# Optimization experiments

Measured on AMD Instinct MI355X. Metric: run time of the kernel, lower is better.

Reference implementation:

```python
import jax, jax.numpy as jnp
import numpy as np

BN_EPS = 1e-5

def conv1x1(w, b, x):
    # w: [O, C], b: [O], x: [B, C, H, W] -> [B, O, H, W]
    return jnp.einsum('oc,bchw->bohw', w, x) + b[None, :, None, None]

def setup_inputs() -> dict:
    key = jax.random.key(0)
    ks = jax.random.split(key, 11)
    C, inter = 256, 128
    B, H, W = 16, 64, 32
    s = 0.05
    return {
        'x': jax.random.normal(ks[0], (B, C, H, W), jnp.float32),
        'g_w': jax.random.normal(ks[1], (inter, C), jnp.float32) * s,
        'g_b': jax.random.normal(ks[2], (inter,), jnp.float32) * s,
        'theta_w': jax.random.normal(ks[3], (inter, C), jnp.float32) * s,
        'theta_b': jax.random.normal(ks[4], (inter,), jnp.float32) * s,
        'phi_w': jax.random.normal(ks[5], (inter, C), jnp.float32) * s,
        'phi_b': jax.random.normal(ks[6], (inter,), jnp.float32) * s,
        'W_w': jax.random.normal(ks[7], (C, inter), jnp.float32) * s,
        'W_b': jax.random.normal(ks[8], (C,), jnp.float32) * s,
        'bn_gamma': jax.random.normal(ks[9], (C,), jnp.float32) * s,
        'bn_beta': jax.random.normal(ks[10], (C,), jnp.float32) * s,
    }

def reference(x, g_w, g_b, theta_w, theta_b, phi_w, phi_b, W_w, W_b, bn_gamma, bn_beta):
    B, C, H, W = x.shape
    N = H * W
    inter = g_w.shape[0]
    # 1x1 conv projections, flattened to token sequences
    g_x = conv1x1(g_w, g_b, x).reshape(B, inter, N).transpose(0, 2, 1)        # [B, N, inter]
    theta_x = conv1x1(theta_w, theta_b, x).reshape(B, inter, N).transpose(0, 2, 1)  # [B, N, inter]
    phi_x = conv1x1(phi_w, phi_b, x).reshape(B, inter, N)                      # [B, inter, N]
    # non-local attention: f = theta @ phi / N, then y = f @ g
    f_div_c = jnp.einsum('bnd,bdm->bnm', theta_x, phi_x) / N                   # [B, N, N]
    y = jnp.einsum('bnm,bmd->bnd', f_div_c, g_x)                               # [B, N, inter]
    y = y.transpose(0, 2, 1).reshape(B, inter, H, W)
    # W: 1x1 conv + BatchNorm (training-mode batch statistics)
    z = conv1x1(W_w, W_b, y)                                                   # [B, C, H, W]
    mean = jnp.mean(z, axis=(0, 2, 3), keepdims=True)
    var = jnp.var(z, axis=(0, 2, 3), keepdims=True)
    z_hat = (z - mean) * jax.lax.rsqrt(var + BN_EPS)
    z_bn = z_hat * bn_gamma[None, :, None, None] + bn_beta[None, :, None, None]
    return z_bn + x
```

## Files before the change

kernel.cpp:

```cpp
#include <hip/hip_runtime.h>

typedef unsigned int uint;
typedef unsigned short ushort;
typedef __attribute__((ext_vector_type(8))) short bf16x8;
typedef __attribute__((ext_vector_type(4))) float f32x4;

#define BB 16
#define CC 256
#define II 128
#define NN 2048
#define BN_EPS 1e-5f

#define OFF_GPART 0
#define OFF_SPART 8388608
#define OFF_GPT   8421376
#define OFF_CP    8425472
#define OFF_STATP 8429568
#define OFF_STAT2 8560640
#define OFF_PT    8561152
#define OFF_R1    8561408
#define OFF_WGB   8561664
#define OFF_ALPHA 8561920
#define OFF_L1    8562176
#define OFF_R2    8566272
#define OFF_FEND  8570368
#define UGRAM 0
#define UE    1048576
#define UFT   1114112
#define USBF  1179648
#define UXT   2228224
#define UZ    10616832

static __device__ __forceinline__ ushort f2bf(float f) {
    uint u = __float_as_uint(f);
    return (ushort)((u + 0x7FFFu + ((u >> 16) & 1u)) >> 16);
}
static __device__ __forceinline__ uint pack2(float a, float b) {
    return (uint)f2bf(a) | ((uint)f2bf(b) << 16);
}
static __device__ __forceinline__ float bflo(uint w) { return __uint_as_float(w << 16); }
static __device__ __forceinline__ float bfhi(uint w) { return __uint_as_float(w & 0xFFFF0000u); }

#define MICRO_FMA(av, bv) \
    acc[0][0] += av.x * bv.x; acc[0][1] += av.x * bv.y; acc[0][2] += av.x * bv.z; acc[0][3] += av.x * bv.w; \
    acc[1][0] += av.y * bv.x; acc[1][1] += av.y * bv.y; acc[1][2] += av.y * bv.z; acc[1][3] += av.y * bv.w; \
    acc[2][0] += av.z * bv.x; acc[2][1] += av.z * bv.y; acc[2][2] += av.z * bv.z; acc[2][3] += av.z * bv.w; \
    acc[3][0] += av.w * bv.x; acc[3][1] += av.w * bv.y; acc[3][2] += av.w * bv.z; acc[3][3] += av.w * bv.w;

__global__ __launch_bounds__(256) void mega1(
    const float* __restrict__ x,
    const float* __restrict__ Ww, const float* __restrict__ Gw,
    const float* __restrict__ Pw, const float* __restrict__ Tw,
    const float* __restrict__ gb, const float* __restrict__ pb, const float* __restrict__ tb,
    float* __restrict__ gpart, float* __restrict__ sPart, ushort* __restrict__ xT,
    ushort* __restrict__ EBF, ushort* __restrict__ FT,
    float* __restrict__ pt, float* __restrict__ r1, float* __restrict__ wgb,
    float* __restrict__ alpha)
{
    __shared__ __align__(16) char smem[20480];
    const int bid = blockIdx.x;
    const int t = threadIdx.x;

    if (bid < 512) {
        ushort (*As)[40] = (ushort(*)[40])smem;
        ushort (*Bs)[40] = (ushort(*)[40])(smem + 10240);
        const int jt = bid & 1, it = (bid >> 1) & 1;
        const int z = bid >> 2;
        const int b = z >> 3, kc = z & 7;
        const int iBase = it * 128, jBase = jt * 128;
        const bool diag = (it == jt);
        const int arow = t >> 1, ah = t & 1;
        const float* aSrc = x + ((size_t)(b * CC + iBase + arow)) * NN + kc * 256 + ah * 16;
        const float* bSrc = x + ((size_t)(b * CC + jBase + arow)) * NN + kc * 256 + ah * 16;
        const int lane = t & 63, wid = t >> 6;
        const int mb = (wid >> 1) * 64, nb = (wid & 1) * 64;
        const int lm = lane & 15, q = lane >> 4;
        f32x4 acc[4][4] = {};
        float ssum = 0.f;

        for (int it16 = 0; it16 < 8; ++it16) {
            const float4* ap = (const float4*)(aSrc + it16 * 32);
            float4 a0 = ap[0], a1 = ap[1], a2 = ap[2], a3 = ap[3];
            uint4 pa0 = { pack2(a0.x,a0.y), pack2(a0.z,a0.w), pack2(a1.x,a1.y), pack2(a1.z,a1.w) };
            uint4 pa1 = { pack2(a2.x,a2.y), pack2(a2.z,a2.w), pack2(a3.x,a3.y), pack2(a3.z,a3.w) };
            *(uint4*)&As[arow][ah * 16]     = pa0;
            *(uint4*)&As[arow][ah * 16 + 8] = pa1;
            if (!diag) {
                const float4* bp = (const float4*)(bSrc + it16 * 32);
                float4 b0 = bp[0], b1 = bp[1], b2 = bp[2], b3 = bp[3];
                uint4 pb0 = { pack2(b0.x,b0.y), pack2(b0.z,b0.w), pack2(b1.x,b1.y), pack2(b1.z,b1.w) };
                uint4 pb1 = { pack2(b2.x,b2.y), pack2(b2.z,b2.w), pack2(b3.x,b3.y), pack2(b3.z,b3.w) };
                *(uint4*)&Bs[arow][ah * 16]     = pb0;
                *(uint4*)&Bs[arow][ah * 16 + 8] = pb1;
            }
            if (jt == 0) {
                ssum += a0.x+a0.y+a0.z+a0.w + a1.x+a1.y+a1.z+a1.w
                      + a2.x+a2.y+a2.z+a2.w + a3.x+a3.y+a3.z+a3.w;
            }
            __syncthreads();
            const ushort (*Bsel)[40] = diag ? (const ushort(*)[40])As : (const ushort(*)[40])Bs;
            bf16x8 af[4], bf[4];
            #pragma unroll
            for (int mt = 0; mt < 4; ++mt)
                af[mt] = *(const bf16x8*)&As[mb + mt * 16 + lm][q * 8];
            #pragma unroll
            for (int nt = 0; nt < 4; ++nt)
                bf[nt] = *(const bf16x8*)&Bsel[nb + nt * 16 + lm][q * 8];
            #pragma unroll
            for (int mt = 0; mt < 4; ++mt)
                #pragma unroll
                for (int nt = 0; nt < 4; ++nt)
                    acc[mt][nt] = __builtin_amdgcn_mfma_f32_16x16x32_bf16(af[mt], bf[nt], acc[mt][nt], 0, 0, 0);
            if (diag) {
                const int n_l = t & 31, cg = t >> 5;
                uint qv[8];
                #pragma unroll
                for (int i2 = 0; i2 < 8; ++i2) {
                    ushort lo = As[cg * 16 + 2*i2][n_l];
                    ushort hi = As[cg * 16 + 2*i2 + 1][n_l];
                    qv[i2] = (uint)lo | ((uint)hi << 16);
                }
                const int ng = kc * 256 + it16 * 32 + n_l;
                uint4* op = (uint4*)(xT + ((size_t)(b * NN + ng)) * CC + iBase + cg * 16);
                op[0] = make_uint4(qv[0], qv[1], qv[2], qv[3]);
                op[1] = make_uint4(qv[4], qv[5], qv[6], qv[7]);
            }
            __syncthreads();
        }
        float* gp = gpart + ((size_t)kc * BB + b) * CC * CC;
        #pragma unroll
        for (int mt = 0; mt < 4; ++mt)
            #pragma unroll
            for (int nt = 0; nt < 4; ++nt)
                #pragma unroll
                for (int r = 0; r < 4; ++r) {
                    const int gi = iBase + mb + mt * 16 + q * 4 + r;
                    const int gj = jBase + nb + nt * 16 + lm;
                    gp[(size_t)gi * CC + gj] = acc[mt][nt][r];
                }
        if (jt == 0) {
            const float so = __shfl_xor(ssum, 1);
            if ((t & 1) == 0)
                sPart[((size_t)kc * BB + b) * CC + iBase + arow] = ssum + so;
        }
        return;
    }

    const int bz = bid - 512;
    if (bz == 32) {
        float ptv = 0.f, r1v = 0.f, wgbv = 0.f;
        for (int d = 0; d < II; ++d) {
            ptv  += Pw[(size_t)d * CC + t] * tb[d];
            r1v  += Tw[(size_t)d * CC + t] * pb[d];
            wgbv += Ww[(size_t)t * II + d] * gb[d];
        }
        pt[t] = ptv; r1[t] = r1v; wgb[t] = wgbv;
        if (t == 0) {
            float al = 0.f;
            for (int d = 0; d < II; ++d) al += pb[d] * tb[d];
            alpha[0] = al;
        }
        return;
    }
    float (*As)[68] = (float(*)[68])smem;
    float (*Bs)[68] = (float(*)[68])(smem + 8704);
    const int a_r = t >> 2, a_k = (t & 3) * 8;
    const int b_n = t & 63, b_k = t >> 6;
    const int ty = t >> 4, tx = t & 15;
    float acc[4][4] = {};
    if (bz < 16) {
        const int cBase = (bz >> 2) * 64, iBase = (bz & 3) * 64;
        const float* ap0 = Ww + (size_t)(cBase + a_r) * II + a_k;
        const float* bp0 = Gw + iBase + b_n;
        for (int k0 = 0; k0 < II; k0 += 32) {
            #pragma unroll
            for (int j = 0; j < 8; ++j) As[a_k + j][a_r] = ap0[k0 + j];
            #pragma unroll
            for (int kk = 0; kk < 8; ++kk) {
                const int k = b_k + kk * 4;
                Bs[k][b_n] = bp0[(size_t)(k0 + k) * CC];
            }
            __syncthreads();
            #pragma unroll
            for (int k = 0; k < 32; ++k) {
                const float4 av = *(const float4*)&As[k][ty * 4];
                const float4 bv = *(const float4*)&Bs[k][tx * 4];
                MICRO_FMA(av, bv)
            }
            __syncthreads();
        }
        #pragma unroll
        for (int ii = 0; ii < 4; ++ii) {
            uint2 o = { pack2(acc[ii][0], acc[ii][1]), pack2(acc[ii][2], acc[ii][3]) };
            *(uint2*)&EBF[(size_t)(cBase + ty * 4 + ii) * CC + iBase + tx * 4] = o;
        }
    } else {
        const int zz = bz - 16;
        const int jBase = (zz >> 2) * 64, kBase = (zz & 3) * 64;
        const float* ap0 = Tw + jBase + b_n;
        const float* bp0 = Pw + kBase + b_n;
        for (int k0 = 0; k0 < II; k0 += 32) {
            #pragma unroll
            for (int kk = 0; kk < 8; ++kk) {
                const int k = b_k + kk * 4;
                As[k][b_n] = ap0[(size_t)(k0 + k) * CC];
                Bs[k][b_n] = bp0[(size_t)(k0 + k) * CC];
            }
            __syncthreads();
            #pragma unroll
            for (int k = 0; k < 32; ++k) {
                const float4 av = *(const float4*)&As[k][ty * 4];
                const float4 bv = *(const float4*)&Bs[k][tx * 4];
                MICRO_FMA(av, bv)
            }
            __syncthreads();
        }
        const float sc = 1.0f / (float)NN;
        #pragma unroll
        for (int ii = 0; ii < 4; ++ii) {
            uint2 o = { pack2(acc[ii][0]*sc, acc[ii][1]*sc), pack2(acc[ii][2]*sc, acc[ii][3]*sc) };
            *(uint2*)&FT[(size_t)(jBase + ty * 4 + ii) * CC + kBase + tx * 4] = o;
        }
    }
}

__global__ __launch_bounds__(256) void mega2(
    const float* __restrict__ gpart, const float* __restrict__ pt,
    ushort* __restrict__ GramBF, float* __restrict__ Gpt)
{
    __shared__ float ptL[256];
    const int bid = blockIdx.x;
    const int t = threadIdx.x;
    const int i = bid * 256 + t;
    const size_t S = (size_t)BB * CC * CC / 4;
    const float4* p = (const float4*)gpart;
    if (t < 256) ptL[t] = pt[t];
    float4 o = { 0.f, 0.f, 0.f, 0.f };
    #pragma unroll
    for (int k = 0; k < 8; ++k) {
        float4 v = p[i + (size_t)k * S];
        o.x += v.x; o.y += v.y; o.z += v.z; o.w += v.w;
    }
    uint2 pk = { pack2(o.x, o.y), pack2(o.z, o.w) };
    ((uint2*)GramBF)[i] = pk;
    __syncthreads();
    const int lane = t & 63;
    float dot = o.x * ptL[lane * 4] + o.y * ptL[lane * 4 + 1]
              + o.z * ptL[lane * 4 + 2] + o.w * ptL[lane * 4 + 3];
    #pragma unroll
    for (int m = 32; m > 0; m >>= 1) dot += __shfl_xor(dot, m);
    if (lane == 0) {
        const int row = bid * 4 + (t >> 6);
        Gpt[row] = dot;
    }
}

__global__ __launch_bounds__(256) void u_kernel(
    const float* __restrict__ sPart, const float* __restrict__ Gpt,
    const ushort* __restrict__ EBF, const ushort* __restrict__ FT,
    const float* __restrict__ pt, const float* __restrict__ r1,
    const float* __restrict__ wgb, const float* __restrict__ alpha,
    float* __restrict__ cprime, float* __restrict__ L1, float* __restrict__ R2)
{
    const int b = blockIdx.x, t = threadIdx.x;
    __shared__ __align__(16) float sL[256], GptL[256], red[256];
    {
        float s = 0.f;
        #pragma unroll
        for (int kc = 0; kc < 8; ++kc) s += sPart[((size_t)kc * BB + b) * CC + t];
        sL[t] = s;
        GptL[t] = Gpt[b * CC + t];
        red[t] = s * pt[t];
    }
    __syncthreads();
    for (int s = 128; s > 0; s >>= 1) {
        if (t < s) red[t] += red[t + s];
        __syncthreads();
    }
    const float spt = red[0];
    float es = 0.f, eg = 0.f;
    {
        const uint4* ep = (const uint4*)(EBF + (size_t)t * CC);
        #pragma unroll 4
        for (int kk = 0; kk < 32; ++kk) {
            uint4 v = ep[kk]; const int k = kk * 8;
            float e0=bflo(v.x),e1=bfhi(v.x),e2=bflo(v.y),e3=bfhi(v.y);
            float e4=bflo(v.z),e5=bfhi(v.z),e6=bflo(v.w),e7=bfhi(v.w);
            es += e0*sL[k]+e1*sL[k+1]+e2*sL[k+2]+e3*sL[k+3]+e4*sL[k+4]+e5*sL[k+5]+e6*sL[k+6]+e7*sL[k+7];
            eg += e0*GptL[k]+e1*GptL[k+1]+e2*GptL[k+2]+e3*GptL[k+3]+e4*GptL[k+4]+e5*GptL[k+5]+e6*GptL[k+6]+e7*GptL[k+7];
        }
    }
    float r2 = 0.f;
    {
        const uint4* fp = (const uint4*)(FT + (size_t)t * CC);
        #pragma unroll 4
        for (int kk = 0; kk < 32; ++kk) {
            uint4 v = fp[kk]; const int k = kk * 8;
            r2 += bflo(v.x)*sL[k]   + bfhi(v.x)*sL[k+1] + bflo(v.y)*sL[k+2] + bfhi(v.y)*sL[k+3]
                + bflo(v.z)*sL[k+4] + bfhi(v.z)*sL[k+5] + bflo(v.w)*sL[k+6] + bfhi(v.w)*sL[k+7];
        }
    }
    const float al = alpha[0];
    const float wg = wgb[t];
    cprime[b * CC + t] = (eg + al * es + spt * wg) / (float)NN + al * wg;
    L1[b * CC + t] = es / (float)NN;
    R2[b * CC + t] = r2 + r1[t];
}

__global__ __launch_bounds__(256) void sfused(
    const ushort* __restrict__ EBF, const ushort* __restrict__ GramBF,
    const ushort* __restrict__ FT,
    const float* __restrict__ r1, const float* __restrict__ R2,
    const float* __restrict__ L1, const float* __restrict__ wgb,
    ushort* __restrict__ Sbf)
{
    __shared__ ushort As[128][40];
    __shared__ ushort Bs[128][40];
    __shared__ ushort Qs[128][264];
    const int t = threadIdx.x;
    const int b = blockIdx.x >> 2;
    const int ct = (blockIdx.x >> 1) & 1, jt = blockIdx.x & 1;
    const int cBase = ct * 128, jBase = jt * 128;
    const int arow = t >> 1, ah = t & 1;
    const int lane = t & 63, wid = t >> 6;
    const int mb = (wid >> 1) * 64, nb = (wid & 1) * 64;
    const int lm = lane & 15, q = lane >> 4;
    const ushort* aSrc = EBF + (size_t)(cBase + arow) * CC + ah * 16;

    #pragma unroll
    for (int half = 0; half < 2; ++half) {
        const ushort* bSrc = GramBF + ((size_t)b * CC + half * 128 + arow) * CC + ah * 16;
        f32x4 acc[4][4] = {};
        for (int k0 = 0; k0 < CC; k0 += 32) {
            *(uint4*)&As[arow][ah * 16]     = ((const uint4*)(aSrc + k0))[0];
            *(uint4*)&As[arow][ah * 16 + 8] = ((const uint4*)(aSrc + k0))[1];
            *(uint4*)&Bs[arow][ah * 16]     = ((const uint4*)(bSrc + k0))[0];
            *(uint4*)&Bs[arow][ah * 16 + 8] = ((const uint4*)(bSrc + k0))[1];
            __syncthreads();
            bf16x8 af[4], bf[4];
            #pragma unroll
            for (int mt = 0; mt < 4; ++mt)
                af[mt] = *(const bf16x8*)&As[mb + mt * 16 + lm][q * 8];
            #pragma unroll
            for (int nt = 0; nt < 4; ++nt)
                bf[nt] = *(const bf16x8*)&Bs[nb + nt * 16 + lm][q * 8];
            #pragma unroll
            for (int mt = 0; mt < 4; ++mt)
                #pragma unroll
                for (int nt = 0; nt < 4; ++nt)
                    acc[mt][nt] = __builtin_amdgcn_mfma_f32_16x16x32_bf16(af[mt], bf[nt], acc[mt][nt], 0, 0, 0);
            __syncthreads();
        }
        #pragma unroll
        for (int mt = 0; mt < 4; ++mt)
            #pragma unroll
            for (int nt = 0; nt < 4; ++nt)
                #pragma unroll
                for (int r = 0; r < 4; ++r)
                    Qs[mb + mt * 16 + q * 4 + r][half * 128 + nb + nt * 16 + lm] = f2bf(acc[mt][nt][r]);
        __syncthreads();
    }
    f32x4 acc[4][4] = {};
    const ushort* fSrc = FT + (size_t)(jBase + arow) * CC + ah * 16;
    for (int k0 = 0; k0 < CC; k0 += 32) {
        *(uint4*)&Bs[arow][ah * 16]     = ((const uint4*)(fSrc + k0))[0];
        *(uint4*)&Bs[arow][ah * 16 + 8] = ((const uint4*)(fSrc + k0))[1];
        __syncthreads();
        bf16x8 af[4], bf[4];
        #pragma unroll
        for (int mt = 0; mt < 4; ++mt)
            af[mt] = *(const bf16x8*)&Qs[mb + mt * 16 + lm][k0 + q * 8];
        #pragma unroll
        for (int nt = 0; nt < 4; ++nt)
            bf[nt] = *(const bf16x8*)&Bs[nb + nt * 16 + lm][q * 8];
        #pragma unroll
        for (int mt = 0; mt < 4; ++mt)
            #pragma unroll
            for (int nt = 0; nt < 4; ++nt)
                acc[mt][nt] = __builtin_amdgcn_mfma_f32_16x16x32_bf16(af[mt], bf[nt], acc[mt][nt], 0, 0, 0);
        __syncthreads();
    }
    float r1v[4], R2v[4];
    #pragma unroll
    for (int nt = 0; nt < 4; ++nt) {
        const int j = jBase + nb + nt * 16 + lm;
        r1v[nt] = r1[j];
        R2v[nt] = R2[b * CC + j];
    }
    ushort* dst = Sbf + (size_t)b * CC * CC;
    #pragma unroll
    for (int mt = 0; mt < 4; ++mt)
        #pragma unroll
        for (int r = 0; r < 4; ++r) {
            const int c = cBase + mb + mt * 16 + q * 4 + r;
            const float l1v = L1[b * CC + c], wgv = wgb[c];
            #pragma unroll
            for (int nt = 0; nt < 4; ++nt) {
                const int j = jBase + nb + nt * 16 + lm;
                dst[(size_t)c * CC + j] = f2bf(acc[mt][nt][r] + l1v * r1v[nt] + wgv * R2v[nt]);
            }
        }
}

__global__ __launch_bounds__(256) void z_mfma(
    const ushort* __restrict__ Sbf, const ushort* __restrict__ xT,
    const float* __restrict__ cprime, ushort* __restrict__ zbf,
    float* __restrict__ statsPart)
{
    __shared__ ushort As[128][40];
    __shared__ ushort Bs[128][40];
    __shared__ float cpL[128];
    __shared__ float sSum[2][128], sSq[2][128];
    const int t = threadIdx.x;
    const int n0 = blockIdx.x * 128, ct = blockIdx.y * 128, b = blockIdx.z;
    const int arow = t >> 1, ah = t & 1;
    const ushort* aSrc = Sbf + ((size_t)(b * CC + ct + arow)) * CC + ah * 16;
    const ushort* bSrc = xT + ((size_t)(b * NN + n0 + arow)) * CC + ah * 16;
    const int lane = t & 63, wid = t >> 6;
    const int mb = (wid >> 1) * 64, nb = (wid & 1) * 64;
    const int lm = lane & 15, q = lane >> 4;
    f32x4 acc[4][4] = {};

    if (t < 128) cpL[t] = cprime[b * CC + ct + t];

    for (int k0 = 0; k0 < CC; k0 += 32) {
        *(uint4*)&As[arow][ah * 16]     = ((const uint4*)(aSrc + k0))[0];
        *(uint4*)&As[arow][ah * 16 + 8] = ((const uint4*)(aSrc + k0))[1];
        *(uint4*)&Bs[arow][ah * 16]     = ((const uint4*)(bSrc + k0))[0];
        *(uint4*)&Bs[arow][ah * 16 + 8] = ((const uint4*)(bSrc + k0))[1];
        __syncthreads();
        bf16x8 af[4], bf[4];
        #pragma unroll
        for (int mt = 0; mt < 4; ++mt)
            af[mt] = *(const bf16x8*)&As[mb + mt * 16 + lm][q * 8];
        #pragma unroll
        for (int nt = 0; nt < 4; ++nt)
            bf[nt] = *(const bf16x8*)&Bs[nb + nt * 16 + lm][q * 8];
        #pragma unroll
        for (int mt = 0; mt < 4; ++mt)
            #pragma unroll
            for (int nt = 0; nt < 4; ++nt)
                acc[mt][nt] = __builtin_amdgcn_mfma_f32_16x16x32_bf16(af[mt], bf[nt], acc[mt][nt], 0, 0, 0);
        __syncthreads();
    }
    const int nbw = wid & 1;
    #pragma unroll
    for (int mt = 0; mt < 4; ++mt) {
        #pragma unroll
        for (int r = 0; r < 4; ++r) {
            const int cl = mb + mt * 16 + q * 4 + r;
            const int ci = ct + cl;
            const float cp = cpL[cl];
            const size_t zrow = ((size_t)(b * CC + ci)) * NN;
            float s1 = 0.f, q1 = 0.f;
            #pragma unroll
            for (int nt = 0; nt < 4; ++nt) {
                const float val = acc[mt][nt][r] + cp;
                const int tok = n0 + nb + nt * 16 + lm;
                zbf[zrow + tok] = f2bf(val);
                s1 += val; q1 += val * val;
            }
            #pragma unroll
            for (int m = 1; m < 16; m <<= 1) {
                s1 += __shfl_xor(s1, m);
                q1 += __shfl_xor(q1, m);
            }
            if (lm == 0) { sSum[nbw][cl] = s1; sSq[nbw][cl] = q1; }
        }
    }
    __syncthreads();
    if (t < 128) {
        const int slot = blockIdx.z * 16 + blockIdx.x;
        statsPart[(size_t)slot * 512 + ct + t]       = sSum[0][t] + sSum[1][t];
        statsPart[(size_t)slot * 512 + 256 + ct + t] = sSq[0][t] + sSq[1][t];
    }
}

__global__ __launch_bounds__(512) void bn_finalize(
    const float* __restrict__ statsPart, float* __restrict__ stats2)
{
    __shared__ float red[4][128];
    __shared__ float sf[128];
    const int g = blockIdx.x;
    const int t = threadIdx.x;
    const int cl = t & 127, sg = t >> 7;
    const int col = (cl < 64) ? (g * 64 + cl) : (256 + g * 64 + (cl - 64));
    float a = 0.f;
    for (int s = sg * 64; s < sg * 64 + 64; ++s)
        a += statsPart[(size_t)s * 512 + col];
    red[sg][cl] = a;
    __syncthreads();
    if (t < 128) sf[t] = red[0][t] + red[1][t] + red[2][t] + red[3][t];
    __syncthreads();
    if (t < 64) {
        const float cnt = (float)(BB * NN);
        const float mean = sf[t] / cnt;
        const float var = sf[64 + t] / cnt - mean * mean;
        const int c = g * 64 + t;
        stats2[c] = mean;
        stats2[CC + c] = rsqrtf(var + BN_EPS);
    }
}

__global__ __launch_bounds__(256) void bn_apply(
    const ushort* __restrict__ zbf, const float* __restrict__ x,
    float* __restrict__ out, const float* __restrict__ stats2,
    const float* __restrict__ gamma, const float* __restrict__ beta)
{
    const size_t i = (size_t)blockIdx.x * 256 + threadIdx.x;
    const size_t base = i * 8;
    const int c = (int)((base >> 11) & (CC - 1));
    const float mean = stats2[c], istd = stats2[CC + c];
    const float gm = gamma[c] * istd;
    const float bt = beta[c] - mean * gm;
    const uint4 zz = *(const uint4*)(zbf + base);
    const float4 x0 = *(const float4*)(x + base);
    const float4 x1 = *(const float4*)(x + base + 4);
    float4 o0, o1;
    o0.x = bflo(zz.x) * gm + bt + x0.x;  o0.y = bfhi(zz.x) * gm + bt + x0.y;
    o0.z = bflo(zz.y) * gm + bt + x0.z;  o0.w = bfhi(zz.y) * gm + bt + x0.w;
    o1.x = bflo(zz.z) * gm + bt + x1.x;  o1.y = bfhi(zz.z) * gm + bt + x1.y;
    o1.z = bflo(zz.w) * gm + bt + x1.z;  o1.w = bfhi(zz.w) * gm + bt + x1.w;
    *(float4*)(out + base) = o0;
    *(float4*)(out + base + 4) = o1;
}

extern "C" void kernel_launch(void* const* d_in, const int* in_sizes, int n_in,
                              void* d_out, int out_size, void* d_ws, size_t ws_size,
                              hipStream_t stream) {
    const float* x    = (const float*)d_in[0];
    const float* g_w  = (const float*)d_in[1];
    const float* g_b  = (const float*)d_in[2];
    const float* th_w = (const float*)d_in[3];
    const float* th_b = (const float*)d_in[4];
    const float* ph_w = (const float*)d_in[5];
    const float* ph_b = (const float*)d_in[6];
    const float* W_w  = (const float*)d_in[7];
    const float* bn_g = (const float*)d_in[9];
    const float* bn_bt= (const float*)d_in[10];
    float* wsf = (float*)d_ws;
    float* out = (float*)d_out;
    ushort* ub = (ushort*)(wsf + OFF_FEND);

    mega1<<<dim3(545), 256, 0, stream>>>(
        x, W_w, g_w, ph_w, th_w, g_b, ph_b, th_b,
        wsf + OFF_GPART, wsf + OFF_SPART, ub + UXT,
        ub + UE, ub + UFT,
        wsf + OFF_PT, wsf + OFF_R1, wsf + OFF_WGB, wsf + OFF_ALPHA);
    mega2<<<dim3(1024), 256, 0, stream>>>(
        wsf + OFF_GPART, wsf + OFF_PT, ub + UGRAM, wsf + OFF_GPT);
    u_kernel<<<dim3(16), 256, 0, stream>>>(
        wsf + OFF_SPART, wsf + OFF_GPT, ub + UE, ub + UFT,
        wsf + OFF_PT, wsf + OFF_R1, wsf + OFF_WGB, wsf + OFF_ALPHA,
        wsf + OFF_CP, wsf + OFF_L1, wsf + OFF_R2);
    sfused<<<dim3(64), 256, 0, stream>>>(
        ub + UE, ub + UGRAM, ub + UFT,
        wsf + OFF_R1, wsf + OFF_R2, wsf + OFF_L1, wsf + OFF_WGB, ub + USBF);
    z_mfma<<<dim3(16, 2, 16), 256, 0, stream>>>(
        ub + USBF, ub + UXT, wsf + OFF_CP, ub + UZ, wsf + OFF_STATP);
    bn_finalize<<<dim3(4), 512, 0, stream>>>(wsf + OFF_STATP, wsf + OFF_STAT2);
    bn_apply<<<dim3(4096), 256, 0, stream>>>(ub + UZ, x, out, wsf + OFF_STAT2, bn_g, bn_bt);
}
```

Baseline: 193.8 us.

## Double-buffer LDS tiles and prefetch next K-slice into registers in Gram and z GEMMs

The Gram-matrix phase of mega1 and the z_mfma kernel now use two LDS buffers and load the next K-slice from global memory into registers while the current slice is consumed by MFMA. The trailing barrier per iteration is removed and replaced by a single barrier that waits only on LDS counters, so global loads can stay in flight across it. This is meant to hide global-load latency behind compute. The cost is double the shared memory (40 KB in mega1), which may reduce occupancy.

```diff
diff --git a/kernel.cpp b/kernel.cpp
--- a/kernel.cpp
+++ b/kernel.cpp
@@ -10,6 +10,8 @@
 #define II 128
 #define NN 2048
 #define BN_EPS 1e-5f
+
+#define SYNC_LDS() { __builtin_amdgcn_s_waitcnt(0xC07F); __builtin_amdgcn_s_barrier(); }
 
 #define OFF_GPART 0
 #define OFF_SPART 8388608
@@ -57,13 +59,11 @@
     float* __restrict__ pt, float* __restrict__ r1, float* __restrict__ wgb,
     float* __restrict__ alpha)
 {
-    __shared__ __align__(16) char smem[20480];
+    __shared__ __align__(16) char smem[40960];
     const int bid = blockIdx.x;
     const int t = threadIdx.x;
 
     if (bid < 512) {
-        ushort (*As)[40] = (ushort(*)[40])smem;
-        ushort (*Bs)[40] = (ushort(*)[40])(smem + 10240);
         const int jt = bid & 1, it = (bid >> 1) & 1;
         const int z = bid >> 2;
         const int b = z >> 3, kc = z & 7;
@@ -78,26 +78,42 @@
         f32x4 acc[4][4] = {};
         float ssum = 0.f;
 
+        float4 pa0, pa1, pa2, pa3, pb0, pb1, pb2, pb3;
+        {
+            const float4* ap = (const float4*)aSrc;
+            pa0 = ap[0]; pa1 = ap[1]; pa2 = ap[2]; pa3 = ap[3];
+            if (!diag) {
+                const float4* bp = (const float4*)bSrc;
+                pb0 = bp[0]; pb1 = bp[1]; pb2 = bp[2]; pb3 = bp[3];
+            }
+        }
+
         for (int it16 = 0; it16 < 8; ++it16) {
-            const float4* ap = (const float4*)(aSrc + it16 * 32);
-            float4 a0 = ap[0], a1 = ap[1], a2 = ap[2], a3 = ap[3];
-            uint4 pa0 = { pack2(a0.x,a0.y), pack2(a0.z,a0.w), pack2(a1.x,a1.y), pack2(a1.z,a1.w) };
-            uint4 pa1 = { pack2(a2.x,a2.y), pack2(a2.z,a2.w), pack2(a3.x,a3.y), pack2(a3.z,a3.w) };
-            *(uint4*)&As[arow][ah * 16]     = pa0;
-            *(uint4*)&As[arow][ah * 16 + 8] = pa1;
+            ushort (*As)[40] = (ushort(*)[40])(smem + (it16 & 1) * 20480);
+            ushort (*Bs)[40] = (ushort(*)[40])(smem + (it16 & 1) * 20480 + 10240);
+            uint4 qa0 = { pack2(pa0.x,pa0.y), pack2(pa0.z,pa0.w), pack2(pa1.x,pa1.y), pack2(pa1.z,pa1.w) };
+            uint4 qa1 = { pack2(pa2.x,pa2.y), pack2(pa2.z,pa2.w), pack2(pa3.x,pa3.y), pack2(pa3.z,pa3.w) };
+            *(uint4*)&As[arow][ah * 16]     = qa0;
+            *(uint4*)&As[arow][ah * 16 + 8] = qa1;
             if (!diag) {
-                const float4* bp = (const float4*)(bSrc + it16 * 32);
-                float4 b0 = bp[0], b1 = bp[1], b2 = bp[2], b3 = bp[3];
-                uint4 pb0 = { pack2(b0.x,b0.y), pack2(b0.z,b0.w), pack2(b1.x,b1.y), pack2(b1.z,b1.w) };
-                uint4 pb1 = { pack2(b2.x,b2.y), pack2(b2.z,b2.w), pack2(b3.x,b3.y), pack2(b3.z,b3.w) };
-                *(uint4*)&Bs[arow][ah * 16]     = pb0;
-                *(uint4*)&Bs[arow][ah * 16 + 8] = pb1;
+                uint4 qb0 = { pack2(pb0.x,pb0.y), pack2(pb0.z,pb0.w), pack2(pb1.x,pb1.y), pack2(pb1.z,pb1.w) };
+                uint4 qb1 = { pack2(pb2.x,pb2.y), pack2(pb2.z,pb2.w), pack2(pb3.x,pb3.y), pack2(pb3.z,pb3.w) };
+                *(uint4*)&Bs[arow][ah * 16]     = qb0;
+                *(uint4*)&Bs[arow][ah * 16 + 8] = qb1;
             }
             if (jt == 0) {
-                ssum += a0.x+a0.y+a0.z+a0.w + a1.x+a1.y+a1.z+a1.w
-                      + a2.x+a2.y+a2.z+a2.w + a3.x+a3.y+a3.z+a3.w;
-            }
-            __syncthreads();
+                ssum += pa0.x+pa0.y+pa0.z+pa0.w + pa1.x+pa1.y+pa1.z+pa1.w
+                      + pa2.x+pa2.y+pa2.z+pa2.w + pa3.x+pa3.y+pa3.z+pa3.w;
+            }
+            if (it16 < 7) {
+                const float4* ap = (const float4*)(aSrc + (it16 + 1) * 32);
+                pa0 = ap[0]; pa1 = ap[1]; pa2 = ap[2]; pa3 = ap[3];
+                if (!diag) {
+                    const float4* bp = (const float4*)(bSrc + (it16 + 1) * 32);
+                    pb0 = bp[0]; pb1 = bp[1]; pb2 = bp[2]; pb3 = bp[3];
+                }
+            }
+            SYNC_LDS();
             const ushort (*Bsel)[40] = diag ? (const ushort(*)[40])As : (const ushort(*)[40])Bs;
             bf16x8 af[4], bf[4];
             #pragma unroll
@@ -125,7 +141,6 @@
                 op[0] = make_uint4(qv[0], qv[1], qv[2], qv[3]);
                 op[1] = make_uint4(qv[4], qv[5], qv[6], qv[7]);
             }
-            __syncthreads();
         }
         float* gp = gpart + ((size_t)kc * BB + b) * CC * CC;
         #pragma unroll
@@ -407,8 +422,8 @@
     const float* __restrict__ cprime, ushort* __restrict__ zbf,
     float* __restrict__ statsPart)
 {
-    __shared__ ushort As[128][40];
-    __shared__ ushort Bs[128][40];
+    __shared__ ushort As[2][128][40];
+    __shared__ ushort Bs[2][128][40];
     __shared__ float cpL[128];
     __shared__ float sSum[2][128], sSq[2][128];
     const int t = threadIdx.x;
@@ -423,25 +438,33 @@
 
     if (t < 128) cpL[t] = cprime[b * CC + ct + t];
 
-    for (int k0 = 0; k0 < CC; k0 += 32) {
-        *(uint4*)&As[arow][ah * 16]     = ((const uint4*)(aSrc + k0))[0];
-        *(uint4*)&As[arow][ah * 16 + 8] = ((const uint4*)(aSrc + k0))[1];
-        *(uint4*)&Bs[arow][ah * 16]     = ((const uint4*)(bSrc + k0))[0];
-        *(uint4*)&Bs[arow][ah * 16 + 8] = ((const uint4*)(bSrc + k0))[1];
-        __syncthreads();
+    uint4 ra0 = ((const uint4*)aSrc)[0], ra1 = ((const uint4*)aSrc)[1];
+    uint4 rb0 = ((const uint4*)bSrc)[0], rb1 = ((const uint4*)bSrc)[1];
+
+    for (int ki = 0; ki < 8; ++ki) {
+        const int buf = ki & 1;
+        *(uint4*)&As[buf][arow][ah * 16]     = ra0;
+        *(uint4*)&As[buf][arow][ah * 16 + 8] = ra1;
+        *(uint4*)&Bs[buf][arow][ah * 16]     = rb0;
+        *(uint4*)&Bs[buf][arow][ah * 16 + 8] = rb1;
+        if (ki < 7) {
+            const int k0 = (ki + 1) * 32;
+            ra0 = ((const uint4*)(aSrc + k0))[0]; ra1 = ((const uint4*)(aSrc + k0))[1];
+            rb0 = ((const uint4*)(bSrc + k0))[0]; rb1 = ((const uint4*)(bSrc + k0))[1];
+        }
+        SYNC_LDS();
         bf16x8 af[4], bf[4];
         #pragma unroll
         for (int mt = 0; mt < 4; ++mt)
-            af[mt] = *(const bf16x8*)&As[mb + mt * 16 + lm][q * 8];
+            af[mt] = *(const bf16x8*)&As[buf][mb + mt * 16 + lm][q * 8];
         #pragma unroll
         for (int nt = 0; nt < 4; ++nt)
-            bf[nt] = *(const bf16x8*)&Bs[nb + nt * 16 + lm][q * 8];
+            bf[nt] = *(const bf16x8*)&Bs[buf][nb + nt * 16 + lm][q * 8];
         #pragma unroll
         for (int mt = 0; mt < 4; ++mt)
             #pragma unroll
             for (int nt = 0; nt < 4; ++nt)
                 acc[mt][nt] = __builtin_amdgcn_mfma_f32_16x16x32_bf16(af[mt], bf[nt], acc[mt][nt], 0, 0, 0);
-        __syncthreads();
     }
     const int nbw = wid & 1;
     #pragma unroll
```

Result: no change. 191.6 us (-1.1%).
